# Kernel optimization log

Hardware: AMD Instinct MI355X
Metric: run time of the kernel (lower is better)

The kernel has to match this reference:

```python
import jax, jax.numpy as jnp
import numpy as np

B, N = 128, 2048
QUERY_DIM, NODE_DIM, OUT_DIM = 256, 128, 256
LAMBDA_INIT = 0.8
LN_EPS = 1e-5


def setup_inputs() -> dict:
    key = jax.random.key(0)
    ks = jax.random.split(key, 8)
    fp_vec = jax.random.normal(ks[0], (B, QUERY_DIM), dtype=jnp.float32)
    node_mat = jax.random.normal(ks[1], (B, N, NODE_DIM), dtype=jnp.float32)
    mask = jax.random.uniform(ks[2], (B, N)) < 0.75
    s = 1.0 / np.sqrt(QUERY_DIM)
    Wq1 = jax.random.uniform(ks[3], (NODE_DIM, QUERY_DIM), minval=-s, maxval=s, dtype=jnp.float32)
    Wq2 = jax.random.uniform(ks[4], (NODE_DIM, QUERY_DIM), minval=-s, maxval=s, dtype=jnp.float32)
    s2 = 1.0 / np.sqrt(NODE_DIM)
    Wk = jax.random.uniform(ks[5], (NODE_DIM, NODE_DIM), minval=-s2, maxval=s2, dtype=jnp.float32)
    Wv = jax.random.uniform(ks[6], (OUT_DIM, NODE_DIM), minval=-s2, maxval=s2, dtype=jnp.float32)
    lambda_logit = jnp.zeros((1,), dtype=jnp.float32)
    gamma = jnp.ones((OUT_DIM,), dtype=jnp.float32)
    beta = jnp.zeros((OUT_DIM,), dtype=jnp.float32)
    return {"fp_vec": fp_vec, "node_mat": node_mat, "mask": mask,
            "Wq1": Wq1, "Wq2": Wq2, "Wk": Wk, "Wv": Wv,
            "lambda_logit": lambda_logit, "gamma": gamma, "beta": beta}


def reference(fp_vec, node_mat, mask, Wq1, Wq2, Wk, Wv, lambda_logit, gamma, beta):
    node_dim = node_mat.shape[-1]
    inv_scale = 1.0 / jnp.sqrt(jnp.asarray(node_dim, jnp.float32))
    # projections (torch Linear: y = x @ W.T)
    q1 = fp_vec @ Wq1.T            # (B, node_dim)
    q2 = fp_vec @ Wq2.T            # (B, node_dim)
    k = jnp.einsum('bnd,ed->bne', node_mat, Wk)   # (B, N, node_dim)
    v = jnp.einsum('bnd,od->bno', node_mat, Wv)   # (B, N, out_dim)
    # single-query scores over nodes
    s1 = jnp.einsum('bd,bnd->bn', q1, k) * inv_scale
    s2 = jnp.einsum('bd,bnd->bn', q2, k) * inv_scale
    pad = jnp.where(mask, 0.0, -1e9).astype(s1.dtype)  # (B, N)
    A1 = jax.nn.softmax(s1 + pad, axis=-1)
    A2 = jax.nn.softmax(s2 + pad, axis=-1)
    lam = LAMBDA_INIT + jax.nn.sigmoid(lambda_logit) * 0.2  # (1,)
    A_diff = A1 - lam * A2         # dropout inactive (eval)
    z = jnp.einsum('bn,bno->bo', A_diff, v)  # (B, out_dim)
    # LayerNorm
    mu = jnp.mean(z, axis=-1, keepdims=True)
    var = jnp.mean(jnp.square(z - mu), axis=-1, keepdims=True)
    return (z - mu) * jax.lax.rsqrt(var + LN_EPS) * gamma + beta
```

## Files before the change

### kernel.cpp

```cpp
#include <hip/hip_runtime.h>
#include <hip/hip_bf16.h>
#include <math.h>

#define BB 128
#define NN 2048
#define ND 128
#define QD 256
#define OD 256
#define CHUNKS 16
#define ROWS_PER_CHUNK (NN / CHUNKS)
#define TILE_ROWS 16
#define TILES (ROWS_PER_CHUNK / TILE_ROWS)
#define PART_STRIDE 260

#define EXP2F(x) __builtin_amdgcn_exp2f(x)

__global__ __launch_bounds__(128) void proj_kernel(
    const float* __restrict__ fp_vec, const float* __restrict__ Wq1,
    const float* __restrict__ Wq2, const float* __restrict__ Wk,
    float* __restrict__ qk1g, float* __restrict__ qk2g)
{
  __shared__ __align__(16) float fp_s[QD];
  __shared__ float q1_s[ND];
  __shared__ float q2_s[ND];
  const int b = blockIdx.x, t = threadIdx.x;
  fp_s[t]       = fp_vec[b * QD + t];
  fp_s[t + 128] = fp_vec[b * QD + 128 + t];
  __syncthreads();
  float a1 = 0.f, a2 = 0.f;
  const float4* w1p = (const float4*)(Wq1 + t * QD);
  const float4* w2p = (const float4*)(Wq2 + t * QD);
  #pragma unroll 8
  for (int q = 0; q < QD / 4; ++q) {
    float4 wa = w1p[q], wb = w2p[q];
    float4 f = *(const float4*)&fp_s[q * 4];
    a1 += f.x * wa.x + f.y * wa.y + f.z * wa.z + f.w * wa.w;
    a2 += f.x * wb.x + f.y * wb.y + f.z * wb.z + f.w * wb.w;
  }
  q1_s[t] = a1;
  q2_s[t] = a2;
  __syncthreads();
  float k1 = 0.f, k2 = 0.f;
  #pragma unroll 8
  for (int e = 0; e < ND; ++e) {
    float wv = Wk[e * ND + t];
    k1 += q1_s[e] * wv;
    k2 += q2_s[e] * wv;
  }
  const float cscale = 0.08838834764831845f * 1.4426950408889634f;
  qk1g[b * ND + t] = k1 * cscale;
  qk2g[b * ND + t] = k2 * cscale;
}

__global__ __launch_bounds__(256) void attn_kernel(
    const float* __restrict__ node, const int* __restrict__ mask,
    const float* __restrict__ qk1g, const float* __restrict__ qk2g,
    float* __restrict__ part)
{
  const int bid = blockIdx.x;
  const int b = bid >> 4;
  const int c = bid & (CHUNKS - 1);
  const int t = threadIdx.x;
  const int wave = t >> 6;
  const int lane = t & 63;
  const int half = lane >> 5;
  const int hl = lane & 31;

  __shared__ __align__(16) float tile_s[2][TILE_ROWS * ND];
  __shared__ float pad_s[ROWS_PER_CHUNK];
  __shared__ float sl1[4], sl2[4];
  __shared__ __align__(16) float sw1[4][ND], sw2[4][ND];

  const int chunk_row0 = c * ROWS_PER_CHUNK;
  if (t < ROWS_PER_CHUNK)
    pad_s[t] = mask[b * NN + chunk_row0 + t] ? 0.f : -1e9f;

  const float4 qk1 = *(const float4*)(qk1g + b * ND + hl * 4);
  const float4 qk2 = *(const float4*)(qk2g + b * ND + hl * 4);

  const float4* gc = (const float4*)(node + (size_t)b * NN * ND
                                     + (size_t)chunk_row0 * ND);

  {
    float4 a0 = gc[t];
    float4 a1 = gc[t + 256];
    float4* d = (float4*)tile_s[0];
    d[t] = a0;
    d[t + 256] = a1;
  }
  __syncthreads();

  float l1 = 0.f, l2 = 0.f;
  float4 w1 = make_float4(0.f, 0.f, 0.f, 0.f);
  float4 w2 = make_float4(0.f, 0.f, 0.f, 0.f);

  #pragma unroll
  for (int tt = 0; tt < TILES; ++tt) {
    float4 y0, y1;
    if (tt + 1 < TILES) {
      y0 = gc[(tt + 1) * (TILE_ROWS * ND / 4) + t];
      y1 = gc[(tt + 1) * (TILE_ROWS * ND / 4) + t + 256];
    }
    __builtin_amdgcn_sched_barrier(0);

    const float* buf = tile_s[tt & 1];
    #pragma unroll
    for (int i = 0; i < 2; ++i) {
      const int r = 4 * wave + 2 * i + half;
      const float4 x = *(const float4*)&buf[r * ND + hl * 4];
      const float pad = pad_s[tt * TILE_ROWS + r];

      float d1 = x.x * qk1.x + x.y * qk1.y + x.z * qk1.z + x.w * qk1.w;
      float d2 = x.x * qk2.x + x.y * qk2.y + x.z * qk2.z + x.w * qk2.w;
      #pragma unroll
      for (int off = 1; off < 32; off <<= 1) {
        d1 += __shfl_xor(d1, off, 64);
        d2 += __shfl_xor(d2, off, 64);
      }
      const float p1 = EXP2F(d1 + pad);
      const float p2 = EXP2F(d2 + pad);
      l1 += p1;
      l2 += p2;
      w1.x += p1 * x.x; w1.y += p1 * x.y; w1.z += p1 * x.z; w1.w += p1 * x.w;
      w2.x += p2 * x.x; w2.y += p2 * x.y; w2.z += p2 * x.z; w2.w += p2 * x.w;
    }
    __syncthreads();
    if (tt + 1 < TILES) {
      float4* d = (float4*)tile_s[(tt + 1) & 1];
      d[t] = y0;
      d[t + 256] = y1;
    }
    __syncthreads();
  }

  l1 += __shfl_xor(l1, 32, 64);
  l2 += __shfl_xor(l2, 32, 64);
  w1.x += __shfl_xor(w1.x, 32, 64); w1.y += __shfl_xor(w1.y, 32, 64);
  w1.z += __shfl_xor(w1.z, 32, 64); w1.w += __shfl_xor(w1.w, 32, 64);
  w2.x += __shfl_xor(w2.x, 32, 64); w2.y += __shfl_xor(w2.y, 32, 64);
  w2.z += __shfl_xor(w2.z, 32, 64); w2.w += __shfl_xor(w2.w, 32, 64);
  if (half == 0) {
    *(float4*)&sw1[wave][hl * 4] = w1;
    *(float4*)&sw2[wave][hl * 4] = w2;
    if (hl == 0) { sl1[wave] = l1; sl2[wave] = l2; }
  }
  __syncthreads();

  float* po = part + (size_t)bid * PART_STRIDE;
  if (t == 0) {
    po[0] = sl1[0] + sl1[1] + sl1[2] + sl1[3];
    po[1] = sl2[0] + sl2[1] + sl2[2] + sl2[3];
  }
  if (t < ND) {
    po[4 + t]   = sw1[0][t] + sw1[1][t] + sw1[2][t] + sw1[3][t];
    po[132 + t] = sw2[0][t] + sw2[1][t] + sw2[2][t] + sw2[3][t];
  }
}

__global__ __launch_bounds__(256) void finish_kernel(
    const float* __restrict__ part, const float* __restrict__ Wv,
    const float* __restrict__ lambda_logit, const float* __restrict__ gamma,
    const float* __restrict__ beta, float* __restrict__ out)
{
  const int b = blockIdx.x, t = threadIdx.x;
  __shared__ __align__(16) float wd_s[ND];
  __shared__ float red[8];

  const float lam = 0.8f + 0.2f / (1.f + __expf(-lambda_logit[0]));
  const float* pb = part + (size_t)b * CHUNKS * PART_STRIDE;

  if (t < ND) {
    float L1 = 0.f, L2 = 0.f, W1 = 0.f, W2 = 0.f;
    #pragma unroll
    for (int i = 0; i < CHUNKS; ++i) {
      const float* pc = pb + (size_t)i * PART_STRIDE;
      L1 += pc[0];
      L2 += pc[1];
      W1 += pc[4 + t];
      W2 += pc[132 + t];
    }
    wd_s[t] = W1 / L1 - lam * (W2 / L2);
  }
  __syncthreads();

  float z = 0.f;
  const float4* wvp = (const float4*)(Wv + t * ND);
  #pragma unroll 8
  for (int d = 0; d < ND / 4; ++d) {
    const float4 w = wvp[d];
    const float4 f = *(const float4*)&wd_s[d * 4];
    z += f.x * w.x + f.y * w.y + f.z * w.z + f.w * w.w;
  }

  const int wave = t >> 6, lane = t & 63;
  float s = z;
  #pragma unroll
  for (int off = 32; off; off >>= 1) s += __shfl_xor(s, off, 64);
  if (lane == 0) red[wave] = s;
  __syncthreads();
  const float mu = (red[0] + red[1] + red[2] + red[3]) * (1.f / OD);
  const float dz = z - mu;
  float vs = dz * dz;
  #pragma unroll
  for (int off = 32; off; off >>= 1) vs += __shfl_xor(vs, off, 64);
  if (lane == 0) red[wave + 4] = vs;
  __syncthreads();
  const float var = (red[4] + red[5] + red[6] + red[7]) * (1.f / OD);
  out[b * OD + t] = dz * rsqrtf(var + 1e-5f) * gamma[t] + beta[t];
}

extern "C" void kernel_launch(void* const* d_in, const int* in_sizes, int n_in,
                              void* d_out, int out_size, void* d_ws, size_t ws_size,
                              hipStream_t stream) {
  const float* fp_vec = (const float*)d_in[0];
  const float* node   = (const float*)d_in[1];
  const int*   mask   = (const int*)d_in[2];
  const float* Wq1    = (const float*)d_in[3];
  const float* Wq2    = (const float*)d_in[4];
  const float* Wk     = (const float*)d_in[5];
  const float* Wv     = (const float*)d_in[6];
  const float* ll     = (const float*)d_in[7];
  const float* gamma  = (const float*)d_in[8];
  const float* beta   = (const float*)d_in[9];
  float* out = (float*)d_out;

  float* qk1g = (float*)d_ws;
  float* qk2g = qk1g + BB * ND;
  float* part = qk2g + BB * ND;

  proj_kernel<<<BB, 128, 0, stream>>>(fp_vec, Wq1, Wq2, Wk, qk1g, qk2g);
  attn_kernel<<<BB * CHUNKS, 256, 0, stream>>>(node, mask, qk1g, qk2g, part);
  finish_kernel<<<BB, 256, 0, stream>>>(part, Wv, ll, gamma, beta, out);
}
```

Measured before the change: 242.0 us.

## Load whole chunk directly to LDS via global_load_lds with more chunks

The attention kernel now issues direct global-to-LDS loads (global_load_lds, 16 bytes per lane) that bring the whole 64-row chunk into shared memory at once. This replaces the register-staged double-buffered tile loop and its per-tile barriers. The grid is doubled to 32 chunks per batch so each block handles fewer rows, which raises parallelism and removes the in-loop synchronisation. The costs are more partial results to combine in the finish kernel and a larger LDS footprint per block (32KB tile), which may limit occupancy.

```diff
diff --git a/kernel.cpp b/kernel.cpp
--- a/kernel.cpp
+++ b/kernel.cpp
@@ -7,13 +7,14 @@
 #define ND 128
 #define QD 256
 #define OD 256
-#define CHUNKS 16
+#define CHUNKS 32
 #define ROWS_PER_CHUNK (NN / CHUNKS)
-#define TILE_ROWS 16
-#define TILES (ROWS_PER_CHUNK / TILE_ROWS)
 #define PART_STRIDE 260
 
 #define EXP2F(x) __builtin_amdgcn_exp2f(x)
+
+typedef __attribute__((address_space(1))) const void gvoid_t;
+typedef __attribute__((address_space(3))) void lvoid_t;
 
 __global__ __launch_bounds__(128) void proj_kernel(
     const float* __restrict__ fp_vec, const float* __restrict__ Wq1,
@@ -58,7 +59,7 @@
     float* __restrict__ part)
 {
   const int bid = blockIdx.x;
-  const int b = bid >> 4;
+  const int b = bid >> 5;
   const int c = bid & (CHUNKS - 1);
   const int t = threadIdx.x;
   const int wave = t >> 6;
@@ -66,7 +67,7 @@
   const int half = lane >> 5;
   const int hl = lane & 31;
 
-  __shared__ __align__(16) float tile_s[2][TILE_ROWS * ND];
+  __shared__ __align__(16) float tile_s[ROWS_PER_CHUNK * ND];
   __shared__ float pad_s[ROWS_PER_CHUNK];
   __shared__ float sl1[4], sl2[4];
   __shared__ __align__(16) float sw1[4][ND], sw2[4][ND];
@@ -75,19 +76,23 @@
   if (t < ROWS_PER_CHUNK)
     pad_s[t] = mask[b * NN + chunk_row0 + t] ? 0.f : -1e9f;
 
+  {
+    const char* gb = (const char*)(node + (size_t)b * NN * ND
+                                   + (size_t)chunk_row0 * ND);
+    const char* gw = gb + wave * 8192 + lane * 16;
+    char* lw = ((char*)tile_s) + wave * 8192;
+    #pragma unroll
+    for (int i = 0; i < 8; ++i) {
+      __builtin_amdgcn_global_load_lds(
+          (gvoid_t*)(gw + i * 1024),
+          (lvoid_t*)(lw + i * 1024),
+          16, 0, 0);
+    }
+  }
+
   const float4 qk1 = *(const float4*)(qk1g + b * ND + hl * 4);
   const float4 qk2 = *(const float4*)(qk2g + b * ND + hl * 4);
 
-  const float4* gc = (const float4*)(node + (size_t)b * NN * ND
-                                     + (size_t)chunk_row0 * ND);
-
-  {
-    float4 a0 = gc[t];
-    float4 a1 = gc[t + 256];
-    float4* d = (float4*)tile_s[0];
-    d[t] = a0;
-    d[t + 256] = a1;
-  }
   __syncthreads();
 
   float l1 = 0.f, l2 = 0.f;
@@ -95,42 +100,24 @@
   float4 w2 = make_float4(0.f, 0.f, 0.f, 0.f);
 
   #pragma unroll
-  for (int tt = 0; tt < TILES; ++tt) {
-    float4 y0, y1;
-    if (tt + 1 < TILES) {
-      y0 = gc[(tt + 1) * (TILE_ROWS * ND / 4) + t];
-      y1 = gc[(tt + 1) * (TILE_ROWS * ND / 4) + t + 256];
+  for (int j = 0; j < 8; ++j) {
+    const int r = 16 * wave + 2 * j + half;
+    const float4 x = *(const float4*)&tile_s[r * ND + hl * 4];
+    const float pad = pad_s[r];
+
+    float d1 = x.x * qk1.x + x.y * qk1.y + x.z * qk1.z + x.w * qk1.w;
+    float d2 = x.x * qk2.x + x.y * qk2.y + x.z * qk2.z + x.w * qk2.w;
+    #pragma unroll
+    for (int off = 1; off < 32; off <<= 1) {
+      d1 += __shfl_xor(d1, off, 64);
+      d2 += __shfl_xor(d2, off, 64);
     }
-    __builtin_amdgcn_sched_barrier(0);
-
-    const float* buf = tile_s[tt & 1];
-    #pragma unroll
-    for (int i = 0; i < 2; ++i) {
-      const int r = 4 * wave + 2 * i + half;
-      const float4 x = *(const float4*)&buf[r * ND + hl * 4];
-      const float pad = pad_s[tt * TILE_ROWS + r];
-
-      float d1 = x.x * qk1.x + x.y * qk1.y + x.z * qk1.z + x.w * qk1.w;
-      float d2 = x.x * qk2.x + x.y * qk2.y + x.z * qk2.z + x.w * qk2.w;
-      #pragma unroll
-      for (int off = 1; off < 32; off <<= 1) {
-        d1 += __shfl_xor(d1, off, 64);
-        d2 += __shfl_xor(d2, off, 64);
-      }
-      const float p1 = EXP2F(d1 + pad);
-      const float p2 = EXP2F(d2 + pad);
-      l1 += p1;
-      l2 += p2;
-      w1.x += p1 * x.x; w1.y += p1 * x.y; w1.z += p1 * x.z; w1.w += p1 * x.w;
-      w2.x += p2 * x.x; w2.y += p2 * x.y; w2.z += p2 * x.z; w2.w += p2 * x.w;
-    }
-    __syncthreads();
-    if (tt + 1 < TILES) {
-      float4* d = (float4*)tile_s[(tt + 1) & 1];
-      d[t] = y0;
-      d[t + 256] = y1;
-    }
-    __syncthreads();
+    const float p1 = EXP2F(d1 + pad);
+    const float p2 = EXP2F(d2 + pad);
+    l1 += p1;
+    l2 += p2;
+    w1.x += p1 * x.x; w1.y += p1 * x.y; w1.z += p1 * x.z; w1.w += p1 * x.w;
+    w2.x += p2 * x.x; w2.y += p2 * x.y; w2.z += p2 * x.z; w2.w += p2 * x.w;
   }
 
   l1 += __shfl_xor(l1, 32, 64);
@@ -171,7 +158,7 @@
 
   if (t < ND) {
     float L1 = 0.f, L2 = 0.f, W1 = 0.f, W2 = 0.f;
-    #pragma unroll
+    #pragma unroll 8
     for (int i = 0; i < CHUNKS; ++i) {
       const float* pc = pb + (size_t)i * PART_STRIDE;
       L1 += pc[0];
```

After: 238.4 us. No clear change (-1.5%).
